# Performance work log

Measured on AMD Instinct MI355X. Metric: run time of the kernel, lower is better.

The kernel has to match this reference:

```python
import jax, jax.numpy as jnp
import numpy as np

B, C, H, W = 256, 1024, 14, 14
C8 = C // 8
TXT = 150 * 1024  # flattened text embed dim
N = H * W  # 196, matches self.l shape (1,196)


def setup_inputs() -> dict:
    key = jax.random.key(0)
    ks = jax.random.split(key, 12)
    s = lambda fan_in: 1.0 / np.sqrt(fan_in)
    return {
        "x": jax.random.normal(ks[0], (B, C, H, W), jnp.float32),
        "text_embed": jax.random.normal(ks[1], (B, 1, 150, 1024), jnp.float32),
        "G_w": jax.random.normal(ks[2], (C, TXT), jnp.float32) * s(TXT),
        "G_b": jnp.zeros((C,), jnp.float32),
        "l": jax.random.normal(ks[3], (1, N), jnp.float32) * 0.02,
        "W_q": jax.random.normal(ks[4], (C8, C), jnp.float32) * s(C),
        "b_q": jnp.zeros((C8,), jnp.float32),
        "W_k": jax.random.normal(ks[5], (C8, C), jnp.float32) * s(C),
        "b_k": jnp.zeros((C8,), jnp.float32),
        "W_v": jax.random.normal(ks[6], (C, C), jnp.float32) * s(C),
        "b_v": jnp.zeros((C,), jnp.float32),
        "gamma": jnp.ones((1,), jnp.float32) * 0.5,
    }


def reference(x, text_embed, G_w, G_b, l, W_q, b_q, W_k, b_k, W_v, b_v, gamma):
    b, c, h, w = x.shape
    n = h * w
    # text preprocessing: squeeze(1) + flatten + Linear G -> (B, C)
    te = text_embed.reshape(b, -1) @ G_w.T + G_b  # (B, C)
    # bmm(te[:, :, None], l broadcast) == outer product per batch -> (B, C, N)
    te_flat = te[:, :, None] * l[None, 0, None, :]  # (B, C, N)
    x_flat = x.reshape(b, c, n)  # (B, C, N)
    # 1x1 convs == channel matmuls
    proj_query = jnp.einsum('qc,bcn->bnq', W_q, x_flat) + b_q  # (B, N, C8)
    proj_key = jnp.einsum('kc,bcn->bkn', W_k, te_flat) + b_k[None, :, None]  # (B, C8, N)
    energy = jnp.einsum('bnq,bqm->bnm', proj_query, proj_key)  # (B, N, N)
    attention = jax.nn.softmax(energy, axis=-1)  # (B, N, N)
    proj_value = jnp.einsum('vc,bcn->bvn', W_v, te_flat) + b_v[None, :, None]  # (B, C, N)
    # out = bmm(value, attention^T): out[b,c,m] = sum_n value[b,c,n] * attn[b,m,n]
    out = jnp.einsum('bcn,bmn->bcm', proj_value, attention)  # (B, C, N)
    out = out.reshape(b, c, h, w)
    return gamma * out + x
```

## Files before the change

kernel.cpp:

```cpp
#include <hip/hip_runtime.h>
#include <hip/hip_bf16.h>

#define BB 256
#define CC 1024
#define CQ 128
#define NN 196
#define TXTK 153600
#define SPLITS 64
#define KCHUNK 2400
#define KSTEPS 75
#define LDP 40

typedef __attribute__((ext_vector_type(8))) short short8;
typedef __attribute__((ext_vector_type(4))) float f32x4;
typedef __attribute__((ext_vector_type(2))) unsigned int u32x2;

static __device__ __forceinline__ unsigned int pkbf(float a, float b) {
  __hip_bfloat162 t = __float22bfloat162_rn(make_float2(a, b));
  unsigned int r;
  __builtin_memcpy(&r, &t, 4);
  return r;
}

static __device__ __forceinline__ float bflo(unsigned int u) {
  unsigned int v = u << 16;
  float f;
  __builtin_memcpy(&f, &v, 4);
  return f;
}
static __device__ __forceinline__ float bfhi(unsigned int u) {
  unsigned int v = u & 0xffff0000u;
  float f;
  __builtin_memcpy(&f, &v, 4);
  return f;
}

__global__ __launch_bounds__(512, 4) void k1_gemm_partial(
    const float* __restrict__ TE, const float* __restrict__ Gw,
    unsigned int* __restrict__ part) {
  __shared__ unsigned short Al[2][128 * LDP];
  __shared__ unsigned short Bl[2][256 * LDP];

  const int tid = threadIdx.x;
  const int fid = blockIdx.x;
  const int sp = fid & 63;
  const int mnt = fid >> 6;
  const int m = mnt >> 2;
  const int nt = mnt & 3;
  const int kbase = sp * KCHUNK;

  const int lane = tid & 63;
  const int w = tid >> 6;
  const int wm = w & 1;
  const int wn = w >> 1;

  const int r0 = tid >> 3;
  const int c0 = (tid & 7) * 4;
  const float* Ap0 = TE + (size_t)(m * 128 + r0) * TXTK + kbase + c0;
  const float* Ap1 = Ap0 + (size_t)64 * TXTK;
  const float* Bp0 = Gw + (size_t)(nt * 256 + r0) * TXTK + kbase + c0;
  const float* Bp1 = Bp0 + (size_t)64 * TXTK;
  const float* Bp2 = Bp0 + (size_t)128 * TXTK;
  const float* Bp3 = Bp0 + (size_t)192 * TXTK;
  const int l0 = r0 * LDP + c0;
  const int l1 = (r0 + 64) * LDP + c0;
  const int l2 = (r0 + 128) * LDP + c0;
  const int l3 = (r0 + 192) * LDP + c0;

  f32x4 ra0, ra1, rb0, rb1, rb2, rb3;
  auto loadRegs = [&](int ko) {
    ra0 = *(const f32x4*)(Ap0 + ko);
    ra1 = *(const f32x4*)(Ap1 + ko);
    rb0 = __builtin_nontemporal_load((const f32x4*)(Bp0 + ko));
    rb1 = __builtin_nontemporal_load((const f32x4*)(Bp1 + ko));
    rb2 = __builtin_nontemporal_load((const f32x4*)(Bp2 + ko));
    rb3 = __builtin_nontemporal_load((const f32x4*)(Bp3 + ko));
  };
  auto cvt4 = [](f32x4 v) {
    uint2 h;
    h.x = pkbf(v.x, v.y);
    h.y = pkbf(v.z, v.w);
    return h;
  };
  auto writeLDS = [&](int buf) {
    *(uint2*)&Al[buf][l0] = cvt4(ra0);
    *(uint2*)&Al[buf][l1] = cvt4(ra1);
    *(uint2*)&Bl[buf][l0] = cvt4(rb0);
    *(uint2*)&Bl[buf][l1] = cvt4(rb1);
    *(uint2*)&Bl[buf][l2] = cvt4(rb2);
    *(uint2*)&Bl[buf][l3] = cvt4(rb3);
  };

  f32x4 acc[4][4];
  const f32x4 z = {0.f, 0.f, 0.f, 0.f};
#pragma unroll
  for (int i = 0; i < 4; ++i)
#pragma unroll
    for (int j = 0; j < 4; ++j) acc[i][j] = z;

  loadRegs(0);
  writeLDS(0);
  __syncthreads();

  const int k8 = (lane >> 4) * 8;
  const int fr = lane & 15;

  for (int ks = 0; ks < KSTEPS; ++ks) {
    const int cur = ks & 1;
    if (ks + 1 < KSTEPS) loadRegs((ks + 1) * 32);

    short8 bfr[4];
#pragma unroll
    for (int ns = 0; ns < 4; ++ns) {
      int col = wn * 64 + ns * 16 + fr;
      bfr[ns] = *(const short8*)&Bl[cur][col * LDP + k8];
    }
#pragma unroll
    for (int ms = 0; ms < 4; ++ms) {
      int row = wm * 64 + ms * 16 + fr;
      short8 af = *(const short8*)&Al[cur][row * LDP + k8];
#pragma unroll
      for (int ns = 0; ns < 4; ++ns)
        acc[ms][ns] = __builtin_amdgcn_mfma_f32_16x16x32_bf16(af, bfr[ns], acc[ms][ns], 0, 0, 0);
    }

    if (ks + 1 < KSTEPS) writeLDS(cur ^ 1);
    __syncthreads();
  }

  u32x2* d2 = (u32x2*)part + (size_t)fid * 8192;
#pragma unroll
  for (int ms = 0; ms < 4; ++ms)
#pragma unroll
    for (int ns = 0; ns < 4; ++ns) {
      u32x2 pk;
      pk.x = pkbf(acc[ms][ns][0], acc[ms][ns][1]);
      pk.y = pkbf(acc[ms][ns][2], acc[ms][ns][3]);
      const int v = ms * 4 + ns;
      __builtin_nontemporal_store(pk, d2 + v * 512 + tid);
    }
}

__global__ __launch_bounds__(1024) void k2_reduce(
    const unsigned int* __restrict__ part, const float* __restrict__ Gb,
    float* __restrict__ te) {
  const int idx = blockIdx.x * 1024 + threadIdx.x;
  const int mnt = idx >> 13;
  const int s = idx & 8191;
  const u32x2* p2 = (const u32x2*)part;

  float a0 = 0.f, a1 = 0.f, a2 = 0.f, a3 = 0.f;
#pragma unroll 4
  for (int sp = 0; sp < SPLITS; ++sp) {
    u32x2 u = __builtin_nontemporal_load(p2 + (size_t)(mnt * 64 + sp) * 8192 + s);
    a0 += bflo(u.x); a1 += bfhi(u.x);
    a2 += bflo(u.y); a3 += bfhi(u.y);
  }

  const int v = s >> 9, t = s & 511;
  const int lane = t & 63, w = t >> 6;
  const int wm = w & 1, wn = w >> 1;
  const int ms = v >> 2, ns = v & 3;
  const int m = mnt >> 2, nt = mnt & 3;
  const int b0 = m * 128 + wm * 64 + ms * 16 + (lane >> 4) * 4;
  const int c = nt * 256 + wn * 64 + ns * 16 + (lane & 15);
  const float gb = Gb[c];
  te[(size_t)(b0 + 0) * CC + c] = a0 + gb;
  te[(size_t)(b0 + 1) * CC + c] = a1 + gb;
  te[(size_t)(b0 + 2) * CC + c] = a2 + gb;
  te[(size_t)(b0 + 3) * CC + c] = a3 + gb;
}

__global__ __launch_bounds__(256) void k3_dual(
    const float* __restrict__ te, const float* __restrict__ Wk,
    const float* __restrict__ Wv, float* __restrict__ kbuf,
    float* __restrict__ vbuf) {
  __shared__ float As[64][33];
  __shared__ float Bs[64][33];
  const int tid = threadIdx.x;
  const int tx = tid & 15, ty = tid >> 4;
  const int bx = blockIdx.x;
  const float* Wt;
  float* outp;
  int Nout, n0;
  if (bx < 2) { Wt = Wk; outp = kbuf; Nout = CQ; n0 = bx * 64; }
  else        { Wt = Wv; outp = vbuf; Nout = CC; n0 = (bx - 2) * 64; }
  const int m0 = blockIdx.y * 64;
  float acc[4][4] = {};
  for (int k0 = 0; k0 < CC; k0 += 32) {
#pragma unroll
    for (int j = 0; j < 2; ++j) {
      int i = tid + 256 * j;
      int r = i >> 3, c4 = (i & 7) * 4;
      f32x4 va = *(const f32x4*)(te + (size_t)(m0 + r) * CC + k0 + c4);
      As[r][c4 + 0] = va.x; As[r][c4 + 1] = va.y; As[r][c4 + 2] = va.z; As[r][c4 + 3] = va.w;
      f32x4 vb4 = *(const f32x4*)(Wt + (size_t)(n0 + r) * CC + k0 + c4);
      Bs[r][c4 + 0] = vb4.x; Bs[r][c4 + 1] = vb4.y; Bs[r][c4 + 2] = vb4.z; Bs[r][c4 + 3] = vb4.w;
    }
    __syncthreads();
#pragma unroll 8
    for (int k = 0; k < 32; ++k) {
      float a[4], bv[4];
#pragma unroll
      for (int i = 0; i < 4; ++i) a[i] = As[ty * 4 + i][k];
#pragma unroll
      for (int j = 0; j < 4; ++j) bv[j] = Bs[tx * 4 + j][k];
#pragma unroll
      for (int i = 0; i < 4; ++i)
#pragma unroll
        for (int j = 0; j < 4; ++j) acc[i][j] += a[i] * bv[j];
    }
    __syncthreads();
  }
#pragma unroll
  for (int i = 0; i < 4; ++i)
#pragma unroll
    for (int j = 0; j < 4; ++j)
      outp[(size_t)(m0 + ty * 4 + i) * Nout + n0 + tx * 4 + j] = acc[i][j];
}

__global__ __launch_bounds__(1024) void k4a_attn(
    const float* __restrict__ x, const float* __restrict__ kb,
    const float* __restrict__ Wq, const float* __restrict__ bq,
    float* __restrict__ pbuf) {
  __shared__ float kbs[CQ];
  __shared__ float wqs[512];
  __shared__ float partl[16][NN];
  __shared__ float dsh;

  const int h = blockIdx.x;
  const int b = blockIdx.y;
  const int ch0 = h * 512;
  const int tid = threadIdx.x;

  if (tid < CQ) kbs[tid] = kb[b * CQ + tid];
  __syncthreads();

  if (tid < 512) {
    float s = 0.f;
#pragma unroll 8
    for (int q = 0; q < CQ; ++q) s += Wq[q * CC + ch0 + tid] * kbs[q];
    wqs[tid] = s;
  }
  if (tid == 1023) {
    float d = 0.f;
    if (h == 0)
      for (int q = 0; q < CQ; ++q) d += bq[q] * kbs[q];
    dsh = d;
  }
  __syncthreads();

  const float* xb = x + (size_t)b * (CC * NN) + (size_t)ch0 * NN;
  if (tid < 784) {
    const int r = tid / 49, n4 = tid % 49;
    f32x4 acc = {0.f, 0.f, 0.f, 0.f};
#pragma unroll 4
    for (int c = r; c < 512; c += 16) {
      f32x4 v = *(const f32x4*)(xb + c * NN + n4 * 4);
      acc += wqs[c] * v;
    }
    partl[r][n4 * 4 + 0] = acc.x;
    partl[r][n4 * 4 + 1] = acc.y;
    partl[r][n4 * 4 + 2] = acc.z;
    partl[r][n4 * 4 + 3] = acc.w;
  }
  __syncthreads();
  if (tid < NN) {
    float s = dsh;
#pragma unroll
    for (int r = 0; r < 16; ++r) s += partl[r][tid];
    pbuf[b * 400 + h * 200 + tid] = s;
  }
}

__global__ __launch_bounds__(256) void k4mid(
    const float* __restrict__ pbuf, const float* __restrict__ l,
    float* __restrict__ sbuf) {
  __shared__ float ls[NN];
  __shared__ float av[NN];
  const int b = blockIdx.x;
  const int tid = threadIdx.x;
  if (tid < NN) {
    ls[tid] = l[tid];
    av[tid] = pbuf[b * 400 + tid] + pbuf[b * 400 + 200 + tid];
  }
  __syncthreads();
  if (tid < NN) {
    const float a = av[tid];
    float m = -1e30f;
    for (int j = 0; j < NN; ++j) m = fmaxf(m, a * ls[j]);
    float num = 0.f, den = 0.f;
    for (int j = 0; j < NN; ++j) {
      float e = __expf(a * ls[j] - m);
      num += ls[j] * e;
      den += e;
    }
    sbuf[b * NN + tid] = num / den;
  }
}

__global__ __launch_bounds__(256) void k4b_epilogue(
    const float* __restrict__ x, const float* __restrict__ vbuf,
    const float* __restrict__ bv, const float* __restrict__ sbuf,
    const float* __restrict__ gammap, float* __restrict__ out) {
  __shared__ __align__(16) float sv[NN];
  __shared__ float Ac[128];
  __shared__ float Bc[128];
  const int sl = blockIdx.x;
  const int b = blockIdx.y;
  const int tid = threadIdx.x;
  const float g = gammap[0];

  if (tid < NN) sv[tid] = sbuf[b * NN + tid];
  if (tid < 128) {
    Ac[tid] = g * vbuf[b * CC + sl * 128 + tid];
    Bc[tid] = g * bv[sl * 128 + tid];
  }
  __syncthreads();

  const float* xb = x + (size_t)b * (CC * NN) + (size_t)sl * 128 * NN;
  float* ob = out + (size_t)b * (CC * NN) + (size_t)sl * 128 * NN;
  for (int f = tid; f < 6272; f += 256) {
    const int c = f / 49;
    const int n4 = f - c * 49;
    f32x4 xv = *(const f32x4*)(xb + f * 4);
    f32x4 s4 = *(const f32x4*)&sv[n4 * 4];
    f32x4 o = Ac[c] * s4 + (Bc[c] + xv);
    __builtin_nontemporal_store(o, (f32x4*)(ob + f * 4));
  }
}

extern "C" void kernel_launch(void* const* d_in, const int* in_sizes, int n_in,
                              void* d_out, int out_size, void* d_ws, size_t ws_size,
                              hipStream_t stream) {
  const float* x    = (const float*)d_in[0];
  const float* TE   = (const float*)d_in[1];
  const float* Gw   = (const float*)d_in[2];
  const float* Gb   = (const float*)d_in[3];
  const float* l    = (const float*)d_in[4];
  const float* Wq   = (const float*)d_in[5];
  const float* bq   = (const float*)d_in[6];
  const float* Wk   = (const float*)d_in[7];
  const float* Wv   = (const float*)d_in[9];
  const float* bv   = (const float*)d_in[10];
  const float* gam  = (const float*)d_in[11];

  float* out  = (float*)d_out;
  unsigned int* part = (unsigned int*)d_out;
  float* te   = (float*)d_ws;
  float* kbuf = te + BB * CC;
  float* vbuf = kbuf + BB * CQ;
  float* sbuf = vbuf + BB * CC;
  float* pbuf = sbuf + BB * NN;

  hipLaunchKernelGGL(k1_gemm_partial, dim3(512), dim3(512), 0, stream, TE, Gw, part);
  hipLaunchKernelGGL(k2_reduce, dim3(64), dim3(1024), 0, stream, part, Gb, te);
  hipLaunchKernelGGL(k3_dual, dim3(18, 4), dim3(256), 0, stream, te, Wk, Wv, kbuf, vbuf);
  hipLaunchKernelGGL(k4a_attn, dim3(2, BB), dim3(1024), 0, stream, x, kbuf, Wq, bq, pbuf);
  hipLaunchKernelGGL(k4mid, dim3(BB), dim3(256), 0, stream, pbuf, l, sbuf);
  hipLaunchKernelGGL(k4b_epilogue, dim3(8, BB), dim3(256), 0, stream, x, vbuf, bv, sbuf, gam, out);
}
```

Measured before the change: 432.0 us.

## Halve GEMM N-tile to double block count and reverse epilogue batch order

The split-K text GEMM now uses 128x128 output tiles instead of 128x256. That doubles the grid to 1024 blocks, halves LDS and accumulator use, and raises the occupancy hint to 5 blocks per SM. Gw loads switch from nontemporal to normal loads, and the reduce kernel's indexing is remapped to the new tile layout. The epilogue walks batches in reverse, apparently to reuse recently touched x/out data in cache. The smaller tile re-reads the TE operand twice as often in exchange for more parallelism and better latency hiding.

```diff
diff --git a/kernel.cpp b/kernel.cpp
--- a/kernel.cpp
+++ b/kernel.cpp
@@ -35,18 +35,18 @@
   return f;
 }
 
-__global__ __launch_bounds__(512, 4) void k1_gemm_partial(
+__global__ __launch_bounds__(512, 5) void k1_gemm_partial(
     const float* __restrict__ TE, const float* __restrict__ Gw,
     unsigned int* __restrict__ part) {
   __shared__ unsigned short Al[2][128 * LDP];
-  __shared__ unsigned short Bl[2][256 * LDP];
+  __shared__ unsigned short Bl[2][128 * LDP];
 
   const int tid = threadIdx.x;
   const int fid = blockIdx.x;
   const int sp = fid & 63;
-  const int mnt = fid >> 6;
-  const int m = mnt >> 2;
-  const int nt = mnt & 3;
+  const int g = fid >> 6;
+  const int m = g >> 3;
+  const int nt = g & 7;
   const int kbase = sp * KCHUNK;
 
   const int lane = tid & 63;
@@ -58,23 +58,17 @@
   const int c0 = (tid & 7) * 4;
   const float* Ap0 = TE + (size_t)(m * 128 + r0) * TXTK + kbase + c0;
   const float* Ap1 = Ap0 + (size_t)64 * TXTK;
-  const float* Bp0 = Gw + (size_t)(nt * 256 + r0) * TXTK + kbase + c0;
+  const float* Bp0 = Gw + (size_t)(nt * 128 + r0) * TXTK + kbase + c0;
   const float* Bp1 = Bp0 + (size_t)64 * TXTK;
-  const float* Bp2 = Bp0 + (size_t)128 * TXTK;
-  const float* Bp3 = Bp0 + (size_t)192 * TXTK;
   const int l0 = r0 * LDP + c0;
   const int l1 = (r0 + 64) * LDP + c0;
-  const int l2 = (r0 + 128) * LDP + c0;
-  const int l3 = (r0 + 192) * LDP + c0;
-
-  f32x4 ra0, ra1, rb0, rb1, rb2, rb3;
+
+  f32x4 ra0, ra1, rb0, rb1;
   auto loadRegs = [&](int ko) {
     ra0 = *(const f32x4*)(Ap0 + ko);
     ra1 = *(const f32x4*)(Ap1 + ko);
-    rb0 = __builtin_nontemporal_load((const f32x4*)(Bp0 + ko));
-    rb1 = __builtin_nontemporal_load((const f32x4*)(Bp1 + ko));
-    rb2 = __builtin_nontemporal_load((const f32x4*)(Bp2 + ko));
-    rb3 = __builtin_nontemporal_load((const f32x4*)(Bp3 + ko));
+    rb0 = *(const f32x4*)(Bp0 + ko);
+    rb1 = *(const f32x4*)(Bp1 + ko);
   };
   auto cvt4 = [](f32x4 v) {
     uint2 h;
@@ -87,16 +81,14 @@
     *(uint2*)&Al[buf][l1] = cvt4(ra1);
     *(uint2*)&Bl[buf][l0] = cvt4(rb0);
     *(uint2*)&Bl[buf][l1] = cvt4(rb1);
-    *(uint2*)&Bl[buf][l2] = cvt4(rb2);
-    *(uint2*)&Bl[buf][l3] = cvt4(rb3);
   };
 
-  f32x4 acc[4][4];
+  f32x4 acc[4][2];
   const f32x4 z = {0.f, 0.f, 0.f, 0.f};
 #pragma unroll
   for (int i = 0; i < 4; ++i)
 #pragma unroll
-    for (int j = 0; j < 4; ++j) acc[i][j] = z;
+    for (int j = 0; j < 2; ++j) acc[i][j] = z;
 
   loadRegs(0);
   writeLDS(0);
@@ -109,10 +101,10 @@
     const int cur = ks & 1;
     if (ks + 1 < KSTEPS) loadRegs((ks + 1) * 32);
 
-    short8 bfr[4];
-#pragma unroll
-    for (int ns = 0; ns < 4; ++ns) {
-      int col = wn * 64 + ns * 16 + fr;
+    short8 bfr[2];
+#pragma unroll
+    for (int ns = 0; ns < 2; ++ns) {
+      int col = wn * 32 + ns * 16 + fr;
       bfr[ns] = *(const short8*)&Bl[cur][col * LDP + k8];
     }
 #pragma unroll
@@ -120,7 +112,7 @@
       int row = wm * 64 + ms * 16 + fr;
       short8 af = *(const short8*)&Al[cur][row * LDP + k8];
 #pragma unroll
-      for (int ns = 0; ns < 4; ++ns)
+      for (int ns = 0; ns < 2; ++ns)
         acc[ms][ns] = __builtin_amdgcn_mfma_f32_16x16x32_bf16(af, bfr[ns], acc[ms][ns], 0, 0, 0);
     }
 
@@ -128,15 +120,15 @@
     __syncthreads();
   }
 
-  u32x2* d2 = (u32x2*)part + (size_t)fid * 8192;
+  u32x2* d2 = (u32x2*)part + (size_t)fid * 4096;
 #pragma unroll
   for (int ms = 0; ms < 4; ++ms)
 #pragma unroll
-    for (int ns = 0; ns < 4; ++ns) {
+    for (int ns = 0; ns < 2; ++ns) {
       u32x2 pk;
       pk.x = pkbf(acc[ms][ns][0], acc[ms][ns][1]);
       pk.y = pkbf(acc[ms][ns][2], acc[ms][ns][3]);
-      const int v = ms * 4 + ns;
+      const int v = ms * 2 + ns;
       __builtin_nontemporal_store(pk, d2 + v * 512 + tid);
     }
 }
@@ -145,14 +137,14 @@
     const unsigned int* __restrict__ part, const float* __restrict__ Gb,
     float* __restrict__ te) {
   const int idx = blockIdx.x * 1024 + threadIdx.x;
-  const int mnt = idx >> 13;
-  const int s = idx & 8191;
+  const int g = idx >> 12;
+  const int s = idx & 4095;
   const u32x2* p2 = (const u32x2*)part;
 
   float a0 = 0.f, a1 = 0.f, a2 = 0.f, a3 = 0.f;
 #pragma unroll 4
   for (int sp = 0; sp < SPLITS; ++sp) {
-    u32x2 u = __builtin_nontemporal_load(p2 + (size_t)(mnt * 64 + sp) * 8192 + s);
+    u32x2 u = __builtin_nontemporal_load(p2 + (size_t)(g * 64 + sp) * 4096 + s);
     a0 += bflo(u.x); a1 += bfhi(u.x);
     a2 += bflo(u.y); a3 += bfhi(u.y);
   }
@@ -160,10 +152,9 @@
   const int v = s >> 9, t = s & 511;
   const int lane = t & 63, w = t >> 6;
   const int wm = w & 1, wn = w >> 1;
-  const int ms = v >> 2, ns = v & 3;
-  const int m = mnt >> 2, nt = mnt & 3;
-  const int b0 = m * 128 + wm * 64 + ms * 16 + (lane >> 4) * 4;
-  const int c = nt * 256 + wn * 64 + ns * 16 + (lane & 15);
+  const int ms = v >> 1, ns = v & 1;
+  const int b0 = (g >> 3) * 128 + wm * 64 + ms * 16 + (lane >> 4) * 4;
+  const int c = (g & 7) * 128 + wn * 32 + ns * 16 + (lane & 15);
   const float gb = Gb[c];
   te[(size_t)(b0 + 0) * CC + c] = a0 + gb;
   te[(size_t)(b0 + 1) * CC + c] = a1 + gb;
@@ -307,7 +298,7 @@
   __shared__ float Ac[128];
   __shared__ float Bc[128];
   const int sl = blockIdx.x;
-  const int b = blockIdx.y;
+  const int b = 255 - blockIdx.y;
   const int tid = threadIdx.x;
   const float g = gammap[0];
 
@@ -353,7 +344,7 @@
   float* sbuf = vbuf + BB * CC;
   float* pbuf = sbuf + BB * NN;
 
-  hipLaunchKernelGGL(k1_gemm_partial, dim3(512), dim3(512), 0, stream, TE, Gw, part);
+  hipLaunchKernelGGL(k1_gemm_partial, dim3(1024), dim3(512), 0, stream, TE, Gw, part);
   hipLaunchKernelGGL(k2_reduce, dim3(64), dim3(1024), 0, stream, part, Gb, te);
   hipLaunchKernelGGL(k3_dual, dim3(18, 4), dim3(256), 0, stream, te, Wk, Wv, kbuf, vbuf);
   hipLaunchKernelGGL(k4a_attn, dim3(2, BB), dim3(1024), 0, stream, x, kbuf, Wq, bq, pbuf);
```

After: 495.8 us. 1.15x slower.
